# Optimization experiments

Measured on AMD Instinct MI355X. Metric: run time of the kernel, lower is better.

## Reference

```python
import jax, jax.numpy as jnp
import numpy as np

TEMP = 1.0
B, FLAT, K, D = 8, 262144, 256, 4  # FLAT = M*D, M = 65536


def setup_inputs() -> dict:
    key = jax.random.key(0)
    k1, k2 = jax.random.split(key)
    x = jax.random.normal(k1, (B, FLAT), dtype=jnp.float32)
    center = jax.random.normal(k2, (K, D), dtype=jnp.float32)
    return {"x": x, "center": center}


def reference(x, center):
    # Soft vector quantization (Q_type='Soft')
    x_ = x.reshape(x.shape[0], -1, D)                      # [B, M, 4]
    # sim = -||x - c||^2, expanded to avoid [B,M,K,4] intermediate
    x_sq = jnp.sum(x_ * x_, axis=-1, keepdims=True)        # [B, M, 1]
    c_sq = jnp.sum(center * center, axis=-1)               # [K]
    xc = jnp.einsum('bmd,kd->bmk', x_, center)             # [B, M, K]
    sim = -(x_sq - 2.0 * xc + c_sq)                        # [B, M, K]
    smx = jax.nn.softmax(TEMP * sim, axis=-1)              # [B, M, K]
    output = jnp.einsum('bmk,kd->bmd', smx, center)        # [B, M, 4]
    return output.reshape(x.shape)
```

## Files before the change

### kernel.cpp

```cpp
#include <hip/hip_runtime.h>
#include <hip/hip_bf16.h>

#ifndef __has_builtin
#define __has_builtin(x) 0
#endif

typedef __attribute__((ext_vector_type(8))) short short8;
typedef __attribute__((ext_vector_type(4))) float floatx4;

__device__ __forceinline__ float fast_exp2(float x) {
#if __has_builtin(__builtin_amdgcn_exp2f)
    return __builtin_amdgcn_exp2f(x);
#else
    return exp2f(x);
#endif
}
__device__ __forceinline__ float fast_rcp(float x) {
#if __has_builtin(__builtin_amdgcn_rcpf)
    return __builtin_amdgcn_rcpf(x);
#else
    return 1.0f / x;
#endif
}
__device__ __forceinline__ unsigned short bf16_of(float v) {
    union { __hip_bfloat16 b; unsigned short s; } cv;
    cv.b = __float2bfloat16(v);
    return cv.s;
}
__device__ __forceinline__ float bf16_back(unsigned short s) {
    union { __hip_bfloat16 b; unsigned short t; } cv;
    cv.t = s;
    return __bfloat162float(cv.b);
}
__device__ __forceinline__ unsigned bcat(unsigned short lo, unsigned short hi) {
    return (unsigned)lo | ((unsigned)hi << 16);
}
__device__ __forceinline__ unsigned pack_bf16(float a, float b) {
    __hip_bfloat162 h = __float22bfloat162_rn(make_float2(a, b));
    union { __hip_bfloat162 h2; unsigned u; } cv;
    cv.h2 = h;
    return cv.u;
}

#define VQ_K 256
#define BLK  256
#define T    4

__global__ __launch_bounds__(BLK, 6) void vq_mfma(const float* __restrict__ x,
                                                  const float* __restrict__ center,
                                                  float* __restrict__ out) {
    __shared__ uint4 s_a[16 * 64];
    __shared__ uint4 s_v[8 * 64];

    const float L2E = 1.4426950408889634f;

    for (int f = threadIdx.x; f < 1024; f += BLK) {
        int kt = f >> 6, q = (f >> 4) & 3, ml = f & 15;
        int k = kt * 16 + ml;
        float4 c = reinterpret_cast<const float4*>(center)[k];
        float s = 2.0f * L2E;
        float c2f[4] = {s * c.x, s * c.y, s * c.z, s * c.w};
        unsigned short ch[4], cl[4];
#pragma unroll
        for (int d = 0; d < 4; ++d) {
            ch[d] = bf16_of(c2f[d]);
            cl[d] = bf16_of(c2f[d] - bf16_back(ch[d]));
        }
        float b = -L2E * (c.x * c.x + c.y * c.y + c.z * c.z + c.w * c.w);
        unsigned short bh = bf16_of(b);
        unsigned short bl = bf16_of(b - bf16_back(bh));
        uint4 e;
        if (q == 0) {
            e.x = bcat(ch[0], ch[1]); e.y = bcat(ch[2], ch[3]);
            e.z = e.x;                e.w = e.y;
        } else if (q == 1) {
            e.x = bcat(cl[0], cl[1]); e.y = bcat(cl[2], cl[3]);
            e.z = bcat(bh, bl);       e.w = 0;
        } else {
            e.x = e.y = e.z = e.w = 0;
        }
        s_a[f] = e;
    }
    for (int f = threadIdx.x; f < 512; f += BLK) {
        int c = f >> 6, q = (f >> 4) & 3, n = f & 15;
        unsigned rr[4];
#pragma unroll
        for (int r = 0; r < 4; ++r) {
            int j0 = 2 * r, j1 = 2 * r + 1;
            int k0 = 32 * c + (j0 < 4 ? 4 * q + j0 : 16 + 4 * q + j0 - 4);
            int k1 = 32 * c + (j1 < 4 ? 4 * q + j1 : 16 + 4 * q + j1 - 4);
            float v0 = (n < 4) ? center[k0 * 4 + n] : (n == 4 ? 1.f : 0.f);
            float v1 = (n < 4) ? center[k1 * 4 + n] : (n == 4 ? 1.f : 0.f);
            rr[r] = bcat(bf16_of(v0), bf16_of(v1));
        }
        s_v[f] = make_uint4(rr[0], rr[1], rr[2], rr[3]);
    }
    __syncthreads();

    const int lane = threadIdx.x & 63;
    const int wv   = threadIdx.x >> 6;
    const int q    = lane >> 4;
    const int ml   = lane & 15;
    const int mbase = blockIdx.x * (4 * 16 * T) + wv * (16 * T);
    const float4* __restrict__ x4 = reinterpret_cast<const float4*>(x);

    union Frag { uint4 u4; unsigned u[4]; short8 v; };

    Frag B[T];
#pragma unroll
    for (int t = 0; t < T; ++t) {
        float4 xv = x4[mbase + t * 16 + ml];
        unsigned short xh[4], xl[4];
        float xf[4] = {xv.x, xv.y, xv.z, xv.w};
#pragma unroll
        for (int d = 0; d < 4; ++d) {
            xh[d] = bf16_of(xf[d]);
            xl[d] = bf16_of(xf[d] - bf16_back(xh[d]));
        }
        unsigned h01 = bcat(xh[0], xh[1]), h23 = bcat(xh[2], xh[3]);
        unsigned l01 = bcat(xl[0], xl[1]), l23 = bcat(xl[2], xl[3]);
        const unsigned ONE2 = 0x3F803F80u;
        B[t].u[0] = (q <= 1) ? h01 : 0;
        B[t].u[1] = (q <= 1) ? h23 : 0;
        B[t].u[2] = (q == 0) ? l01 : ((q == 1) ? ONE2 : 0);
        B[t].u[3] = (q == 0) ? l23 : 0;
    }

    floatx4 O[T];
#pragma unroll
    for (int t = 0; t < T; ++t) O[t] = (floatx4){0.f, 0.f, 0.f, 0.f};

    const floatx4 Z4 = (floatx4){0.f, 0.f, 0.f, 0.f};

    for (int c = 0; c < 8; ++c) {
        Frag a0, a1, vf;
        a0.u4 = s_a[(2 * c) * 64 + lane];
        a1.u4 = s_a[(2 * c + 1) * 64 + lane];
        vf.u4 = s_v[c * 64 + lane];
#pragma unroll
        for (int t = 0; t < T; ++t) {
            floatx4 S0 = __builtin_amdgcn_mfma_f32_16x16x32_bf16(a0.v, B[t].v, Z4, 0, 0, 0);
            floatx4 S1 = __builtin_amdgcn_mfma_f32_16x16x32_bf16(a1.v, B[t].v, Z4, 0, 0, 0);
            Frag p;
            p.u[0] = pack_bf16(fast_exp2(S0[0]), fast_exp2(S0[1]));
            p.u[1] = pack_bf16(fast_exp2(S0[2]), fast_exp2(S0[3]));
            p.u[2] = pack_bf16(fast_exp2(S1[0]), fast_exp2(S1[1]));
            p.u[3] = pack_bf16(fast_exp2(S1[2]), fast_exp2(S1[3]));
            O[t] = __builtin_amdgcn_mfma_f32_16x16x32_bf16(p.v, vf.v, O[t], 0, 0, 0);
        }
    }

#pragma unroll
    for (int t = 0; t < T; ++t) {
#pragma unroll
        for (int r = 0; r < 4; ++r) {
            float den = __shfl(O[t][r], (lane & 48) + 4, 64);
            float val = O[t][r] * fast_rcp(den);
            int m = mbase + t * 16 + q * 4 + r;
            if (ml < 4) out[m * 4 + ml] = val;
        }
    }
}

extern "C" void kernel_launch(void* const* d_in, const int* in_sizes, int n_in,
                              void* d_out, int out_size, void* d_ws, size_t ws_size,
                              hipStream_t stream) {
    const float* x      = (const float*)d_in[0];
    const float* center = (const float*)d_in[1];
    float* out = (float*)d_out;

    int nvec   = in_sizes[0] / 4;
    int blocks = nvec / (4 * 16 * T);
    vq_mfma<<<blocks, BLK, 0, stream>>>(x, center, out);
}
```

Measured before the change: 84.74 us.

## Precompute center MFMA fragments in a prep kernel and read them from global memory

```diff
diff --git a/kernel.cpp b/kernel.cpp
--- a/kernel.cpp
+++ b/kernel.cpp
@@ -44,19 +44,15 @@
 
 #define VQ_K 256
 #define BLK  256
-#define T    4
+#define T    2
 
-__global__ __launch_bounds__(BLK, 6) void vq_mfma(const float* __restrict__ x,
-                                                  const float* __restrict__ center,
-                                                  float* __restrict__ out) {
-    __shared__ uint4 s_a[16 * 64];
-    __shared__ uint4 s_v[8 * 64];
 
+__global__ void vq_prep(const float* __restrict__ center, uint4* __restrict__ ws) {
     const float L2E = 1.4426950408889634f;
-
-    for (int f = threadIdx.x; f < 1024; f += BLK) {
-        int kt = f >> 6, q = (f >> 4) & 3, ml = f & 15;
-        int k = kt * 16 + ml;
+    int f = blockIdx.x * 256 + threadIdx.x;
+    if (f < 1024) {
+        int q = (f >> 4) & 3, ml = f & 15;
+        int k = (f >> 6) * 16 + ml;
         float4 c = reinterpret_cast<const float4*>(center)[k];
         float s = 2.0f * L2E;
         float c2f[4] = {s * c.x, s * c.y, s * c.z, s * c.w};
@@ -79,10 +75,10 @@
         } else {
             e.x = e.y = e.z = e.w = 0;
         }
-        s_a[f] = e;
-    }
-    for (int f = threadIdx.x; f < 512; f += BLK) {
-        int c = f >> 6, q = (f >> 4) & 3, n = f & 15;
+        ws[f] = e;
+    } else {
+        int g = f - 1024;
+        int c = g >> 6, q = (g >> 4) & 3, n = g & 15;
         unsigned rr[4];
 #pragma unroll
         for (int r = 0; r < 4; ++r) {
@@ -93,16 +89,21 @@
             float v1 = (n < 4) ? center[k1 * 4 + n] : (n == 4 ? 1.f : 0.f);
             rr[r] = bcat(bf16_of(v0), bf16_of(v1));
         }
-        s_v[f] = make_uint4(rr[0], rr[1], rr[2], rr[3]);
+        ws[f] = make_uint4(rr[0], rr[1], rr[2], rr[3]);
     }
-    __syncthreads();
+}
 
+__global__ __launch_bounds__(BLK, 8) void vq_main(const float* __restrict__ x,
+                                                  const uint4* __restrict__ ws,
+                                                  float* __restrict__ out) {
     const int lane = threadIdx.x & 63;
     const int wv   = threadIdx.x >> 6;
     const int q    = lane >> 4;
     const int ml   = lane & 15;
     const int mbase = blockIdx.x * (4 * 16 * T) + wv * (16 * T);
     const float4* __restrict__ x4 = reinterpret_cast<const float4*>(x);
+    const uint4* __restrict__ ta = ws;
+    const uint4* __restrict__ tv = ws + 1024;
 
     union Frag { uint4 u4; unsigned u[4]; short8 v; };
 
@@ -110,8 +111,8 @@
 #pragma unroll
     for (int t = 0; t < T; ++t) {
         float4 xv = x4[mbase + t * 16 + ml];
+        float xf[4] = {xv.x, xv.y, xv.z, xv.w};
         unsigned short xh[4], xl[4];
-        float xf[4] = {xv.x, xv.y, xv.z, xv.w};
 #pragma unroll
         for (int d = 0; d < 4; ++d) {
             xh[d] = bf16_of(xf[d]);
@@ -129,14 +130,13 @@
     floatx4 O[T];
 #pragma unroll
     for (int t = 0; t < T; ++t) O[t] = (floatx4){0.f, 0.f, 0.f, 0.f};
-
     const floatx4 Z4 = (floatx4){0.f, 0.f, 0.f, 0.f};
 
     for (int c = 0; c < 8; ++c) {
         Frag a0, a1, vf;
-        a0.u4 = s_a[(2 * c) * 64 + lane];
-        a1.u4 = s_a[(2 * c + 1) * 64 + lane];
-        vf.u4 = s_v[c * 64 + lane];
+        a0.u4 = ta[(2 * c) * 64 + lane];
+        a1.u4 = ta[(2 * c + 1) * 64 + lane];
+        vf.u4 = tv[c * 64 + lane];
 #pragma unroll
         for (int t = 0; t < T; ++t) {
             floatx4 S0 = __builtin_amdgcn_mfma_f32_16x16x32_bf16(a0.v, B[t].v, Z4, 0, 0, 0);
@@ -168,8 +168,11 @@
     const float* x      = (const float*)d_in[0];
     const float* center = (const float*)d_in[1];
     float* out = (float*)d_out;
+    uint4* ws  = (uint4*)d_ws;
+
+    vq_prep<<<6, 256, 0, stream>>>(center, ws);
 
     int nvec   = in_sizes[0] / 4;
     int blocks = nvec / (4 * 16 * T);
-    vq_mfma<<<blocks, BLK, 0, stream>>>(x, center, out);
+    vq_main<<<blocks, BLK, 0, stream>>>(x, ws, out);
 }
```

Result: no change. 83.36 us (-1.6%).
